# Performance work log

Measured on AMD Instinct MI355X. Metric: run time of the kernel, lower is better.

The kernel has to match this reference:

```python
import jax, jax.numpy as jnp
import numpy as np

# ---- dims (see shape_source) ----
N_NODES = 100_000
N_EDGES = 600_000
N_GRAPHS = 512
N_NODE_FEAT = 90   # atom-type vocabulary
H = 128            # n_hidden_feat
E_FEAT = 256       # n_edge_net_feat
G_FEAT = 128       # n_graph_feat
N_CONV = 3         # n_conv * n_edge_labels, conv_labels = [0,0,0]
SCALE = 0.05


def setup_inputs() -> dict:
    key = jax.random.key(0)
    ks = jax.random.split(key, 16)
    nodes = jax.random.randint(ks[0], (N_NODES,), 0, N_NODE_FEAT)
    edge_sources = jax.random.randint(ks[1], (N_EDGES,), 0, N_NODES)
    edge_targets = jax.random.randint(ks[2], (N_EDGES,), 0, N_NODES)
    graph_indices = jnp.sort(jax.random.randint(ks[3], (N_NODES,), 0, N_GRAPHS))
    node_counts = jnp.maximum(jnp.bincount(graph_indices, length=N_GRAPHS), 1).astype(jnp.float32)

    def rn(k, shape):
        return jax.random.normal(k, shape, jnp.float32) * SCALE

    return {
        "nodes": nodes,
        "edge_sources": edge_sources,
        "edge_targets": edge_targets,
        "graph_indices": graph_indices,
        "node_counts": node_counts,
        # learned parameters
        "embed": rn(ks[4], (N_NODE_FEAT, H)),           # NodeEmbedding table
        "Wg": rn(ks[5], (N_CONV, H, H)),                # gate linear per conv (bias=False)
        "We1": rn(ks[6], (N_CONV, H, E_FEAT)),          # EdgeNetwork layer 1 per conv
        "We2": rn(ks[7], (N_CONV, E_FEAT, H)),          # EdgeNetwork layer 2 per conv
        "Wp": rn(ks[8], (H, H)),                        # LinearPooling
        "Wfc1": rn(ks[9], (H, G_FEAT)), "bfc1": jnp.zeros((G_FEAT,), jnp.float32),
        "Wfc2": rn(ks[10], (G_FEAT, G_FEAT)), "bfc2": jnp.zeros((G_FEAT,), jnp.float32),
        "Wr": rn(ks[11], (G_FEAT, 1)), "br": jnp.zeros((1,), jnp.float32),
    }


def reference(nodes, edge_sources, edge_targets, graph_indices, node_counts,
              embed, Wg, We1, We2, Wp, Wfc1, bfc1, Wfc2, bfc2, Wr, br):
    sp = jax.nn.softplus
    # NodeEmbedding: atom-type lookup -> [N, H]
    x = embed[nodes]
    # Gated graph convolutions: gather -> edge MLP + gate -> scatter-add -> residual
    for i in range(N_CONV):
        z = x[edge_sources]                               # [E, H] gather
        e = sp(z @ We1[i]) @ We2[i]                       # EdgeNetwork (2 layers, no shortcut)
        m = jax.nn.sigmoid(z @ Wg[i]) * sp(e)             # gate * edge_activation(message)
        agg = jax.ops.segment_sum(m, edge_targets, num_segments=N_NODES)  # scatter-add
        x = x + sp(agg)                                   # node_activation + residual
    # LinearPooling (last conv only): per-graph mean of linear(x)
    y = jax.ops.segment_sum(x @ Wp, graph_indices, num_segments=N_GRAPHS) / node_counts[:, None]
    # GraphPooling with n_steps=1: activation only (no batch norm)
    g = sp(y)
    # FullConnection stack (n_fc=2)
    g = sp(g @ Wfc1 + bfc1)
    g = sp(g @ Wfc2 + bfc2)
    return g @ Wr + br
```

## Files before the change

### kernel.cpp

```cpp
#include <hip/hip_runtime.h>
#include <hip/hip_bf16.h>

typedef unsigned short u16;
typedef __attribute__((ext_vector_type(8))) short short8;
typedef __attribute__((ext_vector_type(4))) float f32x4;
typedef __attribute__((ext_vector_type(2))) __bf16 bf16x2;

#define NNODES 100000
#define NEDGES 600000
#define NGRAPHS 512
#define HF 128
#define EF 256
#define XS_LD 136
#define US_LD 264
#define GB 32

__device__ __forceinline__ float bfu(u16 u){ return __uint_as_float(((unsigned)u) << 16); }
__device__ __forceinline__ u16 f2bf(float f){
    unsigned u = __float_as_uint(f);
    unsigned r = (u + 0x7fff + ((u >> 16) & 1)) >> 16;
    return (u16)r;
}
__device__ __forceinline__ unsigned pack2(float a, float b){
    bf16x2 v = { (__bf16)a, (__bf16)b };
    return __builtin_bit_cast(unsigned, v);
}

#if __has_builtin(__builtin_amdgcn_rcpf)
#define RCP1(x) __builtin_amdgcn_rcpf(x)
#else
#define RCP1(x) (1.f / (x))
#endif

__device__ __forceinline__ float sp_f(float x){
    return fmaxf(x, 0.f) + __logf(1.f + __expf(-fabsf(x)));
}
__device__ __forceinline__ float sig_f(float x){
    return RCP1(1.f + __expf(-x));
}
__device__ __forceinline__ float lf(const void* p, long i, bool f32){
    return f32 ? ((const float*)p)[i] : bfu(((const u16*)p)[i]);
}

__device__ __forceinline__ bool is_f32(const void* probe){
    const u16* p = (const u16*)probe;
    int lane = threadIdx.x & 63;
    int c = 0;
#pragma unroll
    for (int i = 0; i < 4; i++) c += (fabsf(bfu(p[lane * 4 + i])) > 1.0f) ? 1 : 0;
#pragma unroll
    for (int off = 32; off; off >>= 1) c += __shfl_xor(c, off, 64);
    return c > 8;
}

__global__ __launch_bounds__(256) void prep_kernel(const void* __restrict__ wg,
                                                   const void* __restrict__ we1,
                                                   const void* __restrict__ we2,
                                                   const void* __restrict__ wp,
                                                   const void* __restrict__ wfc1,
                                                   const void* __restrict__ wfc2,
                                                   u16* __restrict__ pwg,
                                                   u16* __restrict__ pwe1,
                                                   u16* __restrict__ pwe2,
                                                   u16* __restrict__ pwp,
                                                   u16* __restrict__ pf1,
                                                   u16* __restrict__ pf2,
                                                   const int* __restrict__ nodes,
                                                   const void* __restrict__ emb,
                                                   u16* __restrict__ x,
                                                   const int* __restrict__ tgt,
                                                   int* __restrict__ counts){
    int b = blockIdx.x, t = threadIdx.x;
    if (b < 960) {
        bool f32 = is_f32(emb);
        int i = b * 256 + t;
        int c = i / 81920, r = i % 81920;
        const void* src; u16* dst; int N, KN, l;
        if (r < 16384)      { src = wg;  dst = pwg;  N = HF; KN = 16384; l = r; }
        else if (r < 49152) { src = we1; dst = pwe1; N = EF; KN = 32768; l = r - 16384; }
        else                { src = we2; dst = pwe2; N = HF; KN = 32768; l = r - 49152; }
        int j = l & 7, lane = (l >> 3) & 63, rest = l >> 9;
        int NT = N >> 4, nt = rest % NT, kt = rest / NT;
        int k = kt * 32 + (lane >> 4) * 8 + j;
        int n = nt * 16 + (lane & 15);
        long base = (long)c * KN;
        dst[base + l] = f2bf(lf(src, base + (long)k * N + n, f32));
    } else if (b < 1152) {
        bool f32 = is_f32(emb);
        int i = (b - 960) * 256 + t;
        int c = i / 16384, l = i % 16384;
        const void* src = (c == 0) ? wp : (c == 1) ? wfc1 : wfc2;
        u16* dst = (c == 0) ? pwp : (c == 1) ? pf1 : pf2;
        int j = l & 7, lane = (l >> 3) & 63, rest = l >> 9;
        int nt = rest & 7, kt = rest >> 3;
        int k = kt * 32 + (lane >> 4) * 8 + j;
        int n = nt * 16 + (lane & 15);
        dst[l] = f2bf(lf(src, (long)k * HF + n, f32));
    } else if (b < 26152) {
        bool f32 = is_f32(emb);
        int i = (b - 1152) * 256 + t;
        int v = i >> 6, c = i & 63;
        long base = (long)nodes[v] * HF + c * 2;
        ((unsigned*)x)[i] = pack2(lf(emb, base, f32), lf(emb, base + 1, f32));
    } else {
        int e = (b - 26152) * 256 + t;
        if (e < NEDGES) atomicAdd(&counts[tgt[e]], 1);
    }
}

__global__ __launch_bounds__(256) void scan1_kernel(const int* __restrict__ counts,
                                                    int* __restrict__ row_ptr,
                                                    int* __restrict__ bsums){
    __shared__ int s[256];
    int t = threadIdx.x;
    int i = blockIdx.x * 256 + t;
    int v = (i < NNODES) ? counts[i] : 0;
    s[t] = v; __syncthreads();
    for (int off = 1; off < 256; off <<= 1) {
        int a = (t >= off) ? s[t - off] : 0;
        __syncthreads();
        s[t] += a;
        __syncthreads();
    }
    if (i < NNODES) row_ptr[i] = s[t] - v;
    if (t == 255) bsums[blockIdx.x] = s[255];
}

__global__ __launch_bounds__(512) void scan2_kernel(const int* __restrict__ bsums,
                                                    int* __restrict__ boffs, int nb){
    __shared__ int s[512];
    int t = threadIdx.x;
    int v = (t < nb) ? bsums[t] : 0;
    s[t] = v; __syncthreads();
    for (int off = 1; off < 512; off <<= 1) {
        int a = (t >= off) ? s[t - off] : 0;
        __syncthreads();
        s[t] += a;
        __syncthreads();
    }
    if (t < nb) boffs[t] = s[t] - v;
}

__global__ __launch_bounds__(256) void scan3_kernel(int* __restrict__ row_ptr,
                                                    const int* __restrict__ boffs,
                                                    int* __restrict__ cursor){
    int i = blockIdx.x * 256 + threadIdx.x;
    if (i < NNODES) {
        int r = row_ptr[i] + boffs[blockIdx.x];
        row_ptr[i] = r;
        cursor[i]  = r;
    }
}

__global__ __launch_bounds__(256) void fill_kernel(const int* __restrict__ src,
                                                   const int* __restrict__ tgt,
                                                   int* __restrict__ cursor,
                                                   int* __restrict__ es){
    int e = blockIdx.x * 256 + threadIdx.x;
    if (e < NEDGES) {
        int pos = atomicAdd(&cursor[tgt[e]], 1);
        es[pos] = src[e];
    }
}

__global__ __launch_bounds__(256) void conv_mfma(const u16* __restrict__ x,
                                                 const u16* __restrict__ pwg,
                                                 const u16* __restrict__ pwe1,
                                                 const u16* __restrict__ pwe2,
                                                 u16* __restrict__ M){
    __shared__ u16 xs[64 * XS_LD];
    __shared__ u16 us[64 * US_LD];
    const int t = threadIdx.x;
    const int w = t >> 6, lane = t & 63;
    const int quad = lane >> 4, nr = lane & 15;
    const long row0 = (long)blockIdx.x * 64;

    for (int c = t; c < 1024; c += 256) {
        int r = c >> 4, c8 = c & 15;
        long node = row0 + r;
        uint4 v = make_uint4(0u, 0u, 0u, 0u);
        if (node < NNODES) v = *(const uint4*)(x + node * HF + c8 * 8);
        *(uint4*)(&xs[r * XS_LD + c8 * 8]) = v;
    }
    __syncthreads();

    {
        short8 A[4][4];
#pragma unroll
        for (int etl = 0; etl < 4; etl++) {
            int et = w * 4 + etl;
#pragma unroll
            for (int kt = 0; kt < 4; kt++)
                A[etl][kt] = *(const short8*)(pwe1 + (((kt * 16 + et) * 64 + lane) << 3));
        }
#pragma unroll
        for (int nt = 0; nt < 4; nt++) {
            short8 bx[4];
#pragma unroll
            for (int kt = 0; kt < 4; kt++)
                bx[kt] = *(const short8*)(&xs[(nt * 16 + nr) * XS_LD + kt * 32 + quad * 8]);
#pragma unroll
            for (int etl = 0; etl < 4; etl++) {
                f32x4 acc = {0.f, 0.f, 0.f, 0.f};
#pragma unroll
                for (int kt = 0; kt < 4; kt++)
                    acc = __builtin_amdgcn_mfma_f32_16x16x32_bf16(A[etl][kt], bx[kt], acc, 0, 0, 0);
                uint2 d;
                d.x = pack2(sp_f(acc[0]), sp_f(acc[1]));
                d.y = pack2(sp_f(acc[2]), sp_f(acc[3]));
                *(uint2*)(&us[(nt * 16 + nr) * US_LD + (w * 4 + etl) * 16 + quad * 4]) = d;
            }
        }
    }
    __syncthreads();

    {
#pragma unroll
        for (int c = 0; c < 2; c++) {
            int et = w * 2 + c;
            short8 AT[8], AG[4];
#pragma unroll
            for (int kt = 0; kt < 8; kt++)
                AT[kt] = *(const short8*)(pwe2 + (((kt * 8 + et) * 64 + lane) << 3));
#pragma unroll
            for (int kt = 0; kt < 4; kt++)
                AG[kt] = *(const short8*)(pwg + (((kt * 8 + et) * 64 + lane) << 3));
#pragma unroll
            for (int nt = 0; nt < 4; nt++) {
                f32x4 aT = {0.f, 0.f, 0.f, 0.f};
                f32x4 aG = {0.f, 0.f, 0.f, 0.f};
#pragma unroll
                for (int kt = 0; kt < 8; kt++) {
                    short8 bu = *(const short8*)(&us[(nt * 16 + nr) * US_LD + kt * 32 + quad * 8]);
                    aT = __builtin_amdgcn_mfma_f32_16x16x32_bf16(AT[kt], bu, aT, 0, 0, 0);
                }
#pragma unroll
                for (int kt = 0; kt < 4; kt++) {
                    short8 bx = *(const short8*)(&xs[(nt * 16 + nr) * XS_LD + kt * 32 + quad * 8]);
                    aG = __builtin_amdgcn_mfma_f32_16x16x32_bf16(AG[kt], bx, aG, 0, 0, 0);
                }
                long node = row0 + nt * 16 + nr;
                if (node < NNODES) {
                    uint2 d;
                    d.x = pack2(sig_f(aG[0]) * sp_f(aT[0]), sig_f(aG[1]) * sp_f(aT[1]));
                    d.y = pack2(sig_f(aG[2]) * sp_f(aT[2]), sig_f(aG[3]) * sp_f(aT[3]));
                    *(uint2*)(M + node * HF + et * 16 + quad * 4) = d;
                }
            }
        }
    }
}

__global__ __launch_bounds__(256) void agg_kernel(const u16* __restrict__ M,
                                                  const int* __restrict__ row_ptr,
                                                  const int* __restrict__ counts,
                                                  const int* __restrict__ es,
                                                  u16* __restrict__ x){
    int wid = blockIdx.x * 4 + (threadIdx.x >> 6);
    int lane = threadIdx.x & 63;
    long v = (long)wid * 4 + (lane >> 4);
    int l = lane & 15;
    if (v >= NNODES) return;
    int start = row_ptr[v], cnt = counts[v];
    float a0 = 0.f, a1 = 0.f, a2 = 0.f, a3 = 0.f;
    float a4 = 0.f, a5 = 0.f, a6 = 0.f, a7 = 0.f;
    const uint4* Mu = (const uint4*)M;
    for (int e = 0; e < cnt; e++) {
        int s = es[start + e];
        uint4 u = Mu[(long)s * 16 + l];
        a0 += bfu((u16)u.x); a1 += bfu((u16)(u.x >> 16));
        a2 += bfu((u16)u.y); a3 += bfu((u16)(u.y >> 16));
        a4 += bfu((u16)u.z); a5 += bfu((u16)(u.z >> 16));
        a6 += bfu((u16)u.w); a7 += bfu((u16)(u.w >> 16));
    }
    uint4* xu = (uint4*)x;
    uint4 xv = xu[v * 16 + l];
    xv.x = pack2(bfu((u16)xv.x) + sp_f(a0), bfu((u16)(xv.x >> 16)) + sp_f(a1));
    xv.y = pack2(bfu((u16)xv.y) + sp_f(a2), bfu((u16)(xv.y >> 16)) + sp_f(a3));
    xv.z = pack2(bfu((u16)xv.z) + sp_f(a4), bfu((u16)(xv.z >> 16)) + sp_f(a5));
    xv.w = pack2(bfu((u16)xv.w) + sp_f(a6), bfu((u16)(xv.w >> 16)) + sp_f(a7));
    xu[v * 16 + l] = xv;
}

__global__ __launch_bounds__(256) void pool_kernel(const u16* __restrict__ x,
                                                   const int* __restrict__ gidx,
                                                   float* __restrict__ xsum){
    int wave = blockIdx.x * 4 + (threadIdx.x >> 6);
    int lane = threadIdx.x & 63;
    long base = (long)wave * 64;
    if (base >= NNODES) return;
    long end = base + 64; if (end > NNODES) end = NNODES;
    const unsigned* xu = (const unsigned*)x;
    int gcur = gidx[base];
    float a0 = 0.f, a1 = 0.f;
    for (long v = base; v < end; v++) {
        int g = gidx[v];
        if (g != gcur) {
            atomicAdd(&xsum[gcur * HF + lane * 2 + 0], a0);
            atomicAdd(&xsum[gcur * HF + lane * 2 + 1], a1);
            a0 = a1 = 0.f; gcur = g;
        }
        unsigned u = xu[v * 64 + lane];
        a0 += bfu((u16)u);
        a1 += bfu((u16)(u >> 16));
    }
    atomicAdd(&xsum[gcur * HF + lane * 2 + 0], a0);
    atomicAdd(&xsum[gcur * HF + lane * 2 + 1], a1);
}

__global__ __launch_bounds__(256) void head_mfma(const float* __restrict__ xsum,
                                                 const void* __restrict__ ncnt,
                                                 const u16* __restrict__ pwp,
                                                 const u16* __restrict__ pf1,
                                                 const u16* __restrict__ pf2,
                                                 const void* __restrict__ bfc1,
                                                 const void* __restrict__ bfc2,
                                                 const void* __restrict__ Wr,
                                                 const void* __restrict__ br,
                                                 void* __restrict__ out,
                                                 const void* __restrict__ probe){
    __shared__ u16 hibuf[2][GB][136];
    __shared__ u16 lobuf[2][GB][136];
    const int t = threadIdx.x;
    const int w = t >> 6, lane = t & 63;
    const int quad = lane >> 4, nr = lane & 15;
    const bool f32 = is_f32(probe);
    const int g0 = blockIdx.x * GB;

    for (int i = t; i < GB * 64; i += 256) {
        int g = i >> 6, c = (i & 63) * 2;
        float f0 = xsum[(g0 + g) * HF + c], f1 = xsum[(g0 + g) * HF + c + 1];
        u16 h0 = f2bf(f0), h1 = f2bf(f1);
        *(unsigned*)&hibuf[0][g][c] = (unsigned)h0 | ((unsigned)h1 << 16);
        *(unsigned*)&lobuf[0][g][c] = pack2(f0 - bfu(h0), f1 - bfu(h1));
    }
    __syncthreads();

    float rc[2];
#pragma unroll
    for (int nt = 0; nt < 2; nt++) rc[nt] = RCP1(lf(ncnt, g0 + nt * 16 + nr, f32));

    int cur = 0;
    for (int layer = 0; layer < 3; layer++) {
        const u16* pw = (layer == 0) ? pwp : (layer == 1) ? pf1 : pf2;
        const void* bias = (layer == 1) ? bfc1 : bfc2;
        int nxt = cur ^ 1;
#pragma unroll
        for (int c = 0; c < 2; c++) {
            int et = w * 2 + c;
            short8 A[4];
#pragma unroll
            for (int kt = 0; kt < 4; kt++)
                A[kt] = *(const short8*)(pw + (((kt * 8 + et) * 64 + lane) << 3));
#pragma unroll
            for (int nt = 0; nt < 2; nt++) {
                f32x4 acc = {0.f, 0.f, 0.f, 0.f};
#pragma unroll
                for (int kt = 0; kt < 4; kt++) {
                    short8 bh = *(const short8*)(&hibuf[cur][nt * 16 + nr][kt * 32 + quad * 8]);
                    short8 bl = *(const short8*)(&lobuf[cur][nt * 16 + nr][kt * 32 + quad * 8]);
                    acc = __builtin_amdgcn_mfma_f32_16x16x32_bf16(A[kt], bh, acc, 0, 0, 0);
                    acc = __builtin_amdgcn_mfma_f32_16x16x32_bf16(A[kt], bl, acc, 0, 0, 0);
                }
                int feat0 = et * 16 + quad * 4;
                float f[4];
#pragma unroll
                for (int r = 0; r < 4; r++) {
                    float a = (layer == 0) ? acc[r] * rc[nt]
                                           : acc[r] + lf(bias, feat0 + r, f32);
                    f[r] = sp_f(a);
                }
                u16 h[4]; float lo[4];
#pragma unroll
                for (int r = 0; r < 4; r++) { h[r] = f2bf(f[r]); lo[r] = f[r] - bfu(h[r]); }
                uint2 dh, dl;
                dh.x = (unsigned)h[0] | ((unsigned)h[1] << 16);
                dh.y = (unsigned)h[2] | ((unsigned)h[3] << 16);
                dl.x = pack2(lo[0], lo[1]);
                dl.y = pack2(lo[2], lo[3]);
                *(uint2*)&hibuf[nxt][nt * 16 + nr][feat0] = dh;
                *(uint2*)&lobuf[nxt][nt * 16 + nr][feat0] = dl;
            }
        }
        __syncthreads();
        cur = nxt;
    }

    int g = t >> 3, sub = t & 7;
    float p = 0.f;
    for (int k = sub * 16; k < sub * 16 + 16; k++) {
        float v = bfu(hibuf[cur][g][k]) + bfu(lobuf[cur][g][k]);
        p += v * lf(Wr, k, f32);
    }
    p += __shfl_down(p, 4, 64);
    p += __shfl_down(p, 2, 64);
    p += __shfl_down(p, 1, 64);
    if (sub == 0) {
        float res = p + lf(br, 0, f32);
        if (f32) ((float*)out)[g0 + g] = res;
        else     ((u16*)out)[g0 + g]  = f2bf(res);
    }
}

extern "C" void kernel_launch(void* const* d_in, const int* in_sizes, int n_in,
                              void* d_out, int out_size, void* d_ws, size_t ws_size,
                              hipStream_t stream) {
    const int* nodes = (const int*)d_in[0];
    const int* esrc  = (const int*)d_in[1];
    const int* etgt  = (const int*)d_in[2];
    const int* gidx  = (const int*)d_in[3];

    size_t off = 0;
    char* w = (char*)d_ws;
    auto take = [&](size_t bytes) -> void* {
        void* p = w + off;
        off = (off + bytes + 255) & ~(size_t)255;
        return p;
    };

    u16* pwg     = (u16*)take((size_t)3 * HF * HF * 2);
    u16* pwe1    = (u16*)take((size_t)3 * HF * EF * 2);
    u16* pwe2    = (u16*)take((size_t)3 * EF * HF * 2);
    u16* pwp     = (u16*)take((size_t)HF * HF * 2);
    u16* pf1     = (u16*)take((size_t)HF * HF * 2);
    u16* pf2     = (u16*)take((size_t)HF * HF * 2);
    int* counts  = (int*)take((size_t)NNODES * 4);
    int* row_ptr = (int*)take((size_t)NNODES * 4);
    int* cursor  = (int*)take((size_t)NNODES * 4);
    int* es      = (int*)take((size_t)NEDGES * 4);
    int* bsums   = (int*)take(2048);
    int* boffs   = (int*)take(2048);
    float* xsum  = (float*)take((size_t)NGRAPHS * HF * 4);
    u16* x       = (u16*)take((size_t)NNODES * HF * 2);
    u16* M       = (u16*)take((size_t)NNODES * HF * 2);

    hipMemsetAsync(counts, 0, (size_t)NNODES * 4, stream);
    hipMemsetAsync(xsum, 0, (size_t)NGRAPHS * HF * 4, stream);

    prep_kernel<<<28496, 256, 0, stream>>>(d_in[6], d_in[7], d_in[8],
                                           d_in[9], d_in[10], d_in[12],
                                           pwg, pwe1, pwe2, pwp, pf1, pf2,
                                           nodes, d_in[5], x, etgt, counts);

    const int NB_SCAN = (NNODES + 255) / 256;
    const int NB_EDGE = (NEDGES + 255) / 256;
    scan1_kernel<<<NB_SCAN, 256, 0, stream>>>(counts, row_ptr, bsums);
    scan2_kernel<<<1, 512, 0, stream>>>(bsums, boffs, NB_SCAN);
    scan3_kernel<<<NB_SCAN, 256, 0, stream>>>(row_ptr, boffs, cursor);
    fill_kernel<<<NB_EDGE, 256, 0, stream>>>(esrc, etgt, cursor, es);

    const int NBC = (NNODES + 63) / 64;
    for (int c = 0; c < 3; c++) {
        conv_mfma<<<NBC, 256, 0, stream>>>(x,
            pwg  + (size_t)c * HF * HF,
            pwe1 + (size_t)c * HF * EF,
            pwe2 + (size_t)c * EF * HF, M);
        agg_kernel<<<(NNODES + 15) / 16, 256, 0, stream>>>(M, row_ptr, counts, es, x);
    }

    pool_kernel<<<(NNODES + 255) / 256, 256, 0, stream>>>(x, gidx, xsum);
    head_mfma<<<NGRAPHS / GB, 256, 0, stream>>>(xsum, d_in[4], pwp, pf1, pf2,
                                                d_in[11], d_in[13], d_in[14], d_in[15],
                                                d_out, d_in[5]);
}
```

Measured before the change: 452.3 us.

## Fuse embedding into first conv and aggregation into next conv kernels

Moves the embedding lookup from the prep kernel into the first conv kernel, which writes x and the shared-memory tile in one pass. Aggregation for layers 1 and 2 is fused into the following conv kernel, which sums neighbour messages directly into the LDS tile, so the separate agg launch and the x re-read are gone. M is double-buffered so a kernel can read the previous layer's messages while writing new ones. The edge loops are unrolled by two with split accumulators to keep more gathers in flight. The cost is that the fused kernel's gather phase runs with conv-sized blocks and LDS, which may lower occupancy for the latency-bound gather.

```diff
diff --git a/kernel.cpp b/kernel.cpp
--- a/kernel.cpp
+++ b/kernel.cpp
@@ -65,9 +65,7 @@
                                                    u16* __restrict__ pwp,
                                                    u16* __restrict__ pf1,
                                                    u16* __restrict__ pf2,
-                                                   const int* __restrict__ nodes,
                                                    const void* __restrict__ emb,
-                                                   u16* __restrict__ x,
                                                    const int* __restrict__ tgt,
                                                    int* __restrict__ counts){
     int b = blockIdx.x, t = threadIdx.x;
@@ -96,14 +94,8 @@
         int k = kt * 32 + (lane >> 4) * 8 + j;
         int n = nt * 16 + (lane & 15);
         dst[l] = f2bf(lf(src, (long)k * HF + n, f32));
-    } else if (b < 26152) {
-        bool f32 = is_f32(emb);
-        int i = (b - 1152) * 256 + t;
-        int v = i >> 6, c = i & 63;
-        long base = (long)nodes[v] * HF + c * 2;
-        ((unsigned*)x)[i] = pack2(lf(emb, base, f32), lf(emb, base + 1, f32));
     } else {
-        int e = (b - 26152) * 256 + t;
+        int e = (b - 1152) * 256 + t;
         if (e < NEDGES) atomicAdd(&counts[tgt[e]], 1);
     }
 }
@@ -163,26 +155,14 @@
     }
 }
 
-__global__ __launch_bounds__(256) void conv_mfma(const u16* __restrict__ x,
-                                                 const u16* __restrict__ pwg,
-                                                 const u16* __restrict__ pwe1,
-                                                 const u16* __restrict__ pwe2,
-                                                 u16* __restrict__ M){
-    __shared__ u16 xs[64 * XS_LD];
-    __shared__ u16 us[64 * US_LD];
+__device__ __forceinline__ void conv_phases(u16* xs, u16* us,
+                                            const u16* __restrict__ pwg,
+                                            const u16* __restrict__ pwe1,
+                                            const u16* __restrict__ pwe2,
+                                            u16* __restrict__ M, long row0){
     const int t = threadIdx.x;
     const int w = t >> 6, lane = t & 63;
     const int quad = lane >> 4, nr = lane & 15;
-    const long row0 = (long)blockIdx.x * 64;
-
-    for (int c = t; c < 1024; c += 256) {
-        int r = c >> 4, c8 = c & 15;
-        long node = row0 + r;
-        uint4 v = make_uint4(0u, 0u, 0u, 0u);
-        if (node < NNODES) v = *(const uint4*)(x + node * HF + c8 * 8);
-        *(uint4*)(&xs[r * XS_LD + c8 * 8]) = v;
-    }
-    __syncthreads();
 
     {
         short8 A[4][4];
@@ -251,6 +231,99 @@
     }
 }
 
+__global__ __launch_bounds__(256) void conv0_mfma(const int* __restrict__ nodes,
+                                                  const void* __restrict__ emb,
+                                                  u16* __restrict__ x,
+                                                  const u16* __restrict__ pwg,
+                                                  const u16* __restrict__ pwe1,
+                                                  const u16* __restrict__ pwe2,
+                                                  u16* __restrict__ M){
+    __shared__ u16 xs[64 * XS_LD];
+    __shared__ u16 us[64 * US_LD];
+    const int t = threadIdx.x;
+    const long row0 = (long)blockIdx.x * 64;
+    const bool f32 = is_f32(emb);
+
+    for (int i = t; i < 4096; i += 256) {
+        int r = i >> 6, c = i & 63;
+        long node = row0 + r;
+        unsigned d = 0u;
+        if (node < NNODES) {
+            int v = nodes[node];
+            if (f32) {
+                const float* row = (const float*)emb + (long)v * HF + c * 2;
+                d = pack2(row[0], row[1]);
+            } else {
+                d = ((const unsigned*)emb)[(long)v * 64 + c];
+            }
+            ((unsigned*)x)[node * 64 + c] = d;
+        }
+        *(unsigned*)(&xs[r * XS_LD + c * 2]) = d;
+    }
+    __syncthreads();
+    conv_phases(xs, us, pwg, pwe1, pwe2, M, row0);
+}
+
+__global__ __launch_bounds__(256) void convagg_mfma(u16* __restrict__ x,
+                                                    const int* __restrict__ row_ptr,
+                                                    const int* __restrict__ counts,
+                                                    const int* __restrict__ es,
+                                                    const u16* __restrict__ Min,
+                                                    const u16* __restrict__ pwg,
+                                                    const u16* __restrict__ pwe1,
+                                                    const u16* __restrict__ pwe2,
+                                                    u16* __restrict__ Mout){
+    __shared__ u16 xs[64 * XS_LD];
+    __shared__ u16 us[64 * US_LD];
+    const int t = threadIdx.x;
+    const long row0 = (long)blockIdx.x * 64;
+    const int l = t & 15, r = t >> 4;
+    const uint4* Mu = (const uint4*)Min;
+
+    for (int rr = r; rr < 64; rr += 16) {
+        long node = row0 + rr;
+        uint4 xv = make_uint4(0u, 0u, 0u, 0u);
+        if (node < NNODES) {
+            int start = row_ptr[node], cnt = counts[node];
+            float a0=0.f,a1=0.f,a2=0.f,a3=0.f,a4=0.f,a5=0.f,a6=0.f,a7=0.f;
+            float b0=0.f,b1=0.f,b2=0.f,b3=0.f,b4=0.f,b5=0.f,b6=0.f,b7=0.f;
+            int e = 0;
+            for (; e + 1 < cnt; e += 2) {
+                int s0 = es[start + e], s1 = es[start + e + 1];
+                uint4 u0 = Mu[(long)s0 * 16 + l];
+                uint4 u1 = Mu[(long)s1 * 16 + l];
+                a0 += bfu((u16)u0.x); a1 += bfu((u16)(u0.x >> 16));
+                a2 += bfu((u16)u0.y); a3 += bfu((u16)(u0.y >> 16));
+                a4 += bfu((u16)u0.z); a5 += bfu((u16)(u0.z >> 16));
+                a6 += bfu((u16)u0.w); a7 += bfu((u16)(u0.w >> 16));
+                b0 += bfu((u16)u1.x); b1 += bfu((u16)(u1.x >> 16));
+                b2 += bfu((u16)u1.y); b3 += bfu((u16)(u1.y >> 16));
+                b4 += bfu((u16)u1.z); b5 += bfu((u16)(u1.z >> 16));
+                b6 += bfu((u16)u1.w); b7 += bfu((u16)(u1.w >> 16));
+            }
+            if (e < cnt) {
+                int s0 = es[start + e];
+                uint4 u0 = Mu[(long)s0 * 16 + l];
+                a0 += bfu((u16)u0.x); a1 += bfu((u16)(u0.x >> 16));
+                a2 += bfu((u16)u0.y); a3 += bfu((u16)(u0.y >> 16));
+                a4 += bfu((u16)u0.z); a5 += bfu((u16)(u0.z >> 16));
+                a6 += bfu((u16)u0.w); a7 += bfu((u16)(u0.w >> 16));
+            }
+            a0 += b0; a1 += b1; a2 += b2; a3 += b3;
+            a4 += b4; a5 += b5; a6 += b6; a7 += b7;
+            uint4 xo = ((const uint4*)x)[node * 16 + l];
+            xv.x = pack2(bfu((u16)xo.x) + sp_f(a0), bfu((u16)(xo.x >> 16)) + sp_f(a1));
+            xv.y = pack2(bfu((u16)xo.y) + sp_f(a2), bfu((u16)(xo.y >> 16)) + sp_f(a3));
+            xv.z = pack2(bfu((u16)xo.z) + sp_f(a4), bfu((u16)(xo.z >> 16)) + sp_f(a5));
+            xv.w = pack2(bfu((u16)xo.w) + sp_f(a6), bfu((u16)(xo.w >> 16)) + sp_f(a7));
+            ((uint4*)x)[node * 16 + l] = xv;
+        }
+        *(uint4*)(&xs[rr * XS_LD + l * 8]) = xv;
+    }
+    __syncthreads();
+    conv_phases(xs, us, pwg, pwe1, pwe2, Mout, row0);
+}
+
 __global__ __launch_bounds__(256) void agg_kernel(const u16* __restrict__ M,
                                                   const int* __restrict__ row_ptr,
                                                   const int* __restrict__ counts,
@@ -262,17 +335,33 @@
     int l = lane & 15;
     if (v >= NNODES) return;
     int start = row_ptr[v], cnt = counts[v];
-    float a0 = 0.f, a1 = 0.f, a2 = 0.f, a3 = 0.f;
-    float a4 = 0.f, a5 = 0.f, a6 = 0.f, a7 = 0.f;
+    float a0=0.f,a1=0.f,a2=0.f,a3=0.f,a4=0.f,a5=0.f,a6=0.f,a7=0.f;
+    float b0=0.f,b1=0.f,b2=0.f,b3=0.f,b4=0.f,b5=0.f,b6=0.f,b7=0.f;
     const uint4* Mu = (const uint4*)M;
-    for (int e = 0; e < cnt; e++) {
-        int s = es[start + e];
-        uint4 u = Mu[(long)s * 16 + l];
-        a0 += bfu((u16)u.x); a1 += bfu((u16)(u.x >> 16));
-        a2 += bfu((u16)u.y); a3 += bfu((u16)(u.y >> 16));
-        a4 += bfu((u16)u.z); a5 += bfu((u16)(u.z >> 16));
-        a6 += bfu((u16)u.w); a7 += bfu((u16)(u.w >> 16));
-    }
+    int e = 0;
+    for (; e + 1 < cnt; e += 2) {
+        int s0 = es[start + e], s1 = es[start + e + 1];
+        uint4 u0 = Mu[(long)s0 * 16 + l];
+        uint4 u1 = Mu[(long)s1 * 16 + l];
+        a0 += bfu((u16)u0.x); a1 += bfu((u16)(u0.x >> 16));
+        a2 += bfu((u16)u0.y); a3 += bfu((u16)(u0.y >> 16));
+        a4 += bfu((u16)u0.z); a5 += bfu((u16)(u0.z >> 16));
+        a6 += bfu((u16)u0.w); a7 += bfu((u16)(u0.w >> 16));
+        b0 += bfu((u16)u1.x); b1 += bfu((u16)(u1.x >> 16));
+        b2 += bfu((u16)u1.y); b3 += bfu((u16)(u1.y >> 16));
+        b4 += bfu((u16)u1.z); b5 += bfu((u16)(u1.z >> 16));
+        b6 += bfu((u16)u1.w); b7 += bfu((u16)(u1.w >> 16));
+    }
+    if (e < cnt) {
+        int s0 = es[start + e];
+        uint4 u0 = Mu[(long)s0 * 16 + l];
+        a0 += bfu((u16)u0.x); a1 += bfu((u16)(u0.x >> 16));
+        a2 += bfu((u16)u0.y); a3 += bfu((u16)(u0.y >> 16));
+        a4 += bfu((u16)u0.z); a5 += bfu((u16)(u0.z >> 16));
+        a6 += bfu((u16)u0.w); a7 += bfu((u16)(u0.w >> 16));
+    }
+    a0 += b0; a1 += b1; a2 += b2; a3 += b3;
+    a4 += b4; a5 += b5; a6 += b6; a7 += b7;
     uint4* xu = (uint4*)x;
     uint4 xv = xu[v * 16 + l];
     xv.x = pack2(bfu((u16)xv.x) + sp_f(a0), bfu((u16)(xv.x >> 16)) + sp_f(a1));
@@ -432,15 +521,16 @@
     int* boffs   = (int*)take(2048);
     float* xsum  = (float*)take((size_t)NGRAPHS * HF * 4);
     u16* x       = (u16*)take((size_t)NNODES * HF * 2);
-    u16* M       = (u16*)take((size_t)NNODES * HF * 2);
+    u16* M0      = (u16*)take((size_t)NNODES * HF * 2);
+    u16* M1      = (u16*)take((size_t)NNODES * HF * 2);
 
     hipMemsetAsync(counts, 0, (size_t)NNODES * 4, stream);
     hipMemsetAsync(xsum, 0, (size_t)NGRAPHS * HF * 4, stream);
 
-    prep_kernel<<<28496, 256, 0, stream>>>(d_in[6], d_in[7], d_in[8],
-                                           d_in[9], d_in[10], d_in[12],
-                                           pwg, pwe1, pwe2, pwp, pf1, pf2,
-                                           nodes, d_in[5], x, etgt, counts);
+    prep_kernel<<<3496, 256, 0, stream>>>(d_in[6], d_in[7], d_in[8],
+                                          d_in[9], d_in[10], d_in[12],
+                                          pwg, pwe1, pwe2, pwp, pf1, pf2,
+                                          d_in[5], etgt, counts);
 
     const int NB_SCAN = (NNODES + 255) / 256;
     const int NB_EDGE = (NEDGES + 255) / 256;
@@ -450,13 +540,13 @@
     fill_kernel<<<NB_EDGE, 256, 0, stream>>>(esrc, etgt, cursor, es);
 
     const int NBC = (NNODES + 63) / 64;
-    for (int c = 0; c < 3; c++) {
-        conv_mfma<<<NBC, 256, 0, stream>>>(x,
-            pwg  + (size_t)c * HF * HF,
-            pwe1 + (size_t)c * HF * EF,
-            pwe2 + (size_t)c * EF * HF, M);
-        agg_kernel<<<(NNODES + 15) / 16, 256, 0, stream>>>(M, row_ptr, counts, es, x);
-    }
+    conv0_mfma<<<NBC, 256, 0, stream>>>(nodes, d_in[5], x,
+        pwg, pwe1, pwe2, M0);
+    convagg_mfma<<<NBC, 256, 0, stream>>>(x, row_ptr, counts, es, M0,
+        pwg + (size_t)1 * HF * HF, pwe1 + (size_t)1 * HF * EF, pwe2 + (size_t)1 * EF * HF, M1);
+    convagg_mfma<<<NBC, 256, 0, stream>>>(x, row_ptr, counts, es, M1,
+        pwg + (size_t)2 * HF * HF, pwe1 + (size_t)2 * HF * EF, pwe2 + (size_t)2 * EF * HF, M0);
+    agg_kernel<<<(NNODES + 15) / 16, 256, 0, stream>>>(M0, row_ptr, counts, es, x);
 
     pool_kernel<<<(NNODES + 255) / 256, 256, 0, stream>>>(x, gidx, xsum);
     head_mfma<<<NGRAPHS / GB, 256, 0, stream>>>(xsum, d_in[4], pwp, pf1, pf2,
```

Result: slower. 493.5 us (+9.1%).
